# Kernel optimization log

Hardware: AMD Instinct MI355X
Metric: run time of the kernel (lower is better)

## Reference

```python
import jax, jax.numpy as jnp
import numpy as np

HEADS = 8
DIM_HEAD = 64


def setup_inputs() -> dict:
    key = jax.random.key(0)
    ks = jax.random.split(key, 6)
    dim = 512
    inner = HEADS * DIM_HEAD  # 512
    x = jax.random.normal(ks[0], (4, 4096, dim), dtype=jnp.float32)
    s = 1.0 / np.sqrt(dim)
    Wq = jax.random.normal(ks[1], (dim, inner), dtype=jnp.float32) * s
    Wk = jax.random.normal(ks[2], (dim, inner), dtype=jnp.float32) * s
    Wv = jax.random.normal(ks[3], (dim, inner), dtype=jnp.float32) * s
    Wo = jax.random.normal(ks[4], (inner, dim), dtype=jnp.float32) * (1.0 / np.sqrt(inner))
    bo = jax.random.normal(ks[5], (dim,), dtype=jnp.float32) * 0.01
    return {"x": x, "Wq": Wq, "Wk": Wk, "Wv": Wv, "Wo": Wo, "bo": bo}


def reference(x, Wq, Wk, Wv, Wo, bo):
    b, n, _ = x.shape
    h, d = HEADS, DIM_HEAD
    # project and split heads: [b, h, n, d]
    q = (x @ Wq).reshape(b, n, h, d).transpose(0, 2, 1, 3)
    k = (x @ Wk).reshape(b, n, h, d).transpose(0, 2, 1, 3)
    v = (x @ Wv).reshape(b, n, h, d).transpose(0, 2, 1, 3)
    q = jax.nn.softmax(q, axis=-1)
    k = jax.nn.softmax(k, axis=-1)
    context = jnp.einsum('bhnd,bhne->bhde', k, v)  # small d x d per head
    out = jnp.einsum('bhnd,bhde->bhne', q, context)
    out = out.transpose(0, 2, 1, 3).reshape(b, n, h * d)
    return out @ Wo + bo
```

## Files before the change

### kernel.cpp

```cpp
#include <hip/hip_runtime.h>

typedef unsigned short u16;
typedef unsigned int   u32;
typedef __bf16 bf16x8 __attribute__((ext_vector_type(8)));
typedef float  f32x4  __attribute__((ext_vector_type(4)));
typedef u16    u16x8  __attribute__((ext_vector_type(8)));
typedef u16    u16x4  __attribute__((ext_vector_type(4)));

__device__ __forceinline__ float b2f(u16 h) {
  return __builtin_bit_cast(float, ((u32)h) << 16);
}
__device__ __forceinline__ u16 f2b(float f) {
  u32 u = __builtin_bit_cast(u32, f);
  u32 r = u + 0x7FFFu + ((u >> 16) & 1u);
  return (u16)(r >> 16);
}

#define GLD_AS1(p) ((const __attribute__((address_space(1))) void*)(p))
#define LDS_AS3(p) ((__attribute__((address_space(3))) void*)(p))

__global__ void gemm_qkv_kernel(const u16* __restrict__ A, const u16* __restrict__ Bt,
                                u16* __restrict__ qb, u16* __restrict__ kT,
                                u16* __restrict__ vT) {
  const int K = 512;
  __shared__ u16 smem[2 * 64 * 72];
  u16* As = smem;
  u16* Bs = smem + 128 * 32;
  const int id = blockIdx.x;
  const int tn = id >> 7;
  const int tm = (id & 7) * 16 + ((id >> 3) & 15);
  const int tileN = tn * 128;
  const int tileM = tm * 128;
  const int t = threadIdx.x;
  const int lane = t & 63;
  const int wave = t >> 6;
  const int mbase = (wave >> 1) * 64;
  const int nbase = (wave & 1) * 64;
  const int fm = lane & 15;
  const int kg = lane >> 4;

  f32x4 acc[4][4];
#pragma unroll
  for (int i = 0; i < 4; ++i)
#pragma unroll
    for (int j = 0; j < 4; ++j) acc[i][j] = (f32x4){0.f, 0.f, 0.f, 0.f};

  for (int k0 = 0; k0 < K; k0 += 32) {
#pragma unroll
    for (int p = 0; p < 2; ++p) {
      int c = p * 256 + t;
      int r = c >> 2;
      int g = (c & 3) ^ ((r >> 1) & 3);
      const u16* ga = A + (size_t)(tileM + r) * K + (k0 + g * 8);
      __builtin_amdgcn_global_load_lds(GLD_AS1(ga), LDS_AS3(As + c * 8), 16, 0, 0);
      const u16* gb = Bt + (size_t)(tileN + r) * K + (k0 + g * 8);
      __builtin_amdgcn_global_load_lds(GLD_AS1(gb), LDS_AS3(Bs + c * 8), 16, 0, 0);
    }
    __syncthreads();

    bf16x8 af[4], bfr[4];
#pragma unroll
    for (int mi = 0; mi < 4; ++mi) {
      int m = mbase + mi * 16 + fm;
      int sg = kg ^ ((m >> 1) & 3);
      af[mi] = *(const bf16x8*)(As + m * 32 + sg * 8);
    }
#pragma unroll
    for (int ni = 0; ni < 4; ++ni) {
      int n = nbase + ni * 16 + fm;
      int sg = kg ^ ((n >> 1) & 3);
      bfr[ni] = *(const bf16x8*)(Bs + n * 32 + sg * 8);
    }
#pragma unroll
    for (int mi = 0; mi < 4; ++mi)
#pragma unroll
      for (int ni = 0; ni < 4; ++ni)
        acc[mi][ni] = __builtin_amdgcn_mfma_f32_16x16x32_bf16(af[mi], bfr[ni],
                                                              acc[mi][ni], 0, 0, 0);
    __syncthreads();
  }

  const int rq = lane >> 4;
  const int region = tn >> 2;

  float inv[4][4];
  if (region <= 1) {
#pragma unroll
    for (int mi = 0; mi < 4; ++mi)
#pragma unroll
      for (int ni = 0; ni < 4; ++ni)
#pragma unroll
        for (int reg = 0; reg < 4; ++reg)
          acc[mi][ni][reg] = __expf(acc[mi][ni][reg]);
#pragma unroll
    for (int mi = 0; mi < 4; ++mi)
#pragma unroll
      for (int reg = 0; reg < 4; ++reg) {
        float s = acc[mi][0][reg] + acc[mi][1][reg] + acc[mi][2][reg] + acc[mi][3][reg];
        s += __shfl_xor(s, 1);
        s += __shfl_xor(s, 2);
        s += __shfl_xor(s, 4);
        s += __shfl_xor(s, 8);
        inv[mi][reg] = 1.f / s;
      }
  } else {
#pragma unroll
    for (int mi = 0; mi < 4; ++mi)
#pragma unroll
      for (int reg = 0; reg < 4; ++reg) inv[mi][reg] = 1.f;
  }

  if (region == 0) {
#pragma unroll
    for (int mi = 0; mi < 4; ++mi)
#pragma unroll
      for (int ni = 0; ni < 4; ++ni)
#pragma unroll
        for (int reg = 0; reg < 4; ++reg) {
          int gr = tileM + mbase + mi * 16 + rq * 4 + reg;
          int gc = tileN + nbase + ni * 16 + fm;
          qb[(size_t)gr * 512 + gc] = f2b(acc[mi][ni][reg] * inv[mi][reg]);
        }
  }

  u16* scw = smem + (wave & 1) * (64 * 72);
  u16* base = (region == 1) ? kT : vT;
  const int hd = tileN + nbase - ((region == 1) ? 512 : 1024);
  const int gr0 = tileM + mbase;
  const int bh = (gr0 >> 12) * 8 + (hd >> 6);
  const int n0 = gr0 & 4095;

  auto transpose_store = [&]() {
#pragma unroll
    for (int mi = 0; mi < 4; ++mi)
#pragma unroll
      for (int ni = 0; ni < 4; ++ni) {
        u16x4 o;
#pragma unroll
        for (int reg = 0; reg < 4; ++reg)
          o[reg] = f2b(acc[mi][ni][reg] * inv[mi][reg]);
        *(u16x4*)(scw + (ni * 16 + fm) * 72 + mi * 16 + rq * 4) = o;
      }
#pragma unroll
    for (int i = 0; i < 8; ++i) {
      int row = i * 8 + (lane >> 3);
      int seg = lane & 7;
      u16x8 val = *(const u16x8*)(scw + row * 72 + seg * 8);
      *(u16x8*)(base + ((size_t)bh * 64 + row) * 4096 + n0 + seg * 8) = val;
    }
  };

  if (region != 0 && wave < 2) transpose_store();
  __syncthreads();
  if (region != 0 && wave >= 2) transpose_store();
}

__global__ void prep_all_kernel(const float* __restrict__ x, const float* __restrict__ Wq,
                                const float* __restrict__ Wk, const float* __restrict__ Wv,
                                const float* __restrict__ Wo, u16* __restrict__ xb,
                                u16* __restrict__ Wt, u16* __restrict__ Wot) {
  __shared__ u16 tr[64 * 72];
  const int id = blockIdx.x;
  const int t = threadIdx.x;

  if (id < 4096) {
    int i = (id * 256 + t) * 8;
    float4 a = *(const float4*)(x + i);
    float4 b = *(const float4*)(x + i + 4);
    u16x8 o;
    o[0] = f2b(a.x); o[1] = f2b(a.y); o[2] = f2b(a.z); o[3] = f2b(a.w);
    o[4] = f2b(b.x); o[5] = f2b(b.y); o[6] = f2b(b.z); o[7] = f2b(b.w);
    *(u16x8*)(xb + i) = o;
    return;
  }
  const float* W;
  u16* dst;
  int n0, k0;
  if (id < 4288) {
    int tile = id - 4096;
    n0 = (tile >> 3) * 64;
    k0 = (tile & 7) * 64;
    W = (n0 < 512) ? Wq : ((n0 < 1024) ? Wk : Wv);
    dst = Wt;
  } else {
    int tile = id - 4288;
    n0 = (tile >> 3) * 64;
    k0 = (tile & 7) * 64;
    W = Wo;
    dst = Wot;
  }
  int cin = (n0 & 511);
  int c = t & 63;
  int r0 = t >> 6;
#pragma unroll
  for (int i = 0; i < 16; ++i) {
    int r = r0 * 16 + i;
    tr[c * 72 + r] = f2b(W[(size_t)(k0 + r) * 512 + cin + c]);
  }
  __syncthreads();
#pragma unroll
  for (int j = 0; j < 2; ++j) {
    int idx = j * 256 + t;
    int row = idx >> 3;
    int seg = idx & 7;
    u16x8 val = *(const u16x8*)(tr + row * 72 + seg * 8);
    *(u16x8*)(dst + (size_t)(n0 + row) * 512 + k0 + seg * 8) = val;
  }
}

__global__ void context_kernel(const u16* __restrict__ kT, const u16* __restrict__ vT,
                               float* __restrict__ ctxp) {
  __shared__ u16 ks_lds[64 * 32];
  __shared__ u16 vs_lds[64 * 32];
  const int bh = blockIdx.x;
  const int s = blockIdx.y;
  const int t = threadIdx.x;
  const int lane = t & 63;
  const int wave = t >> 6;
  const int fm = lane & 15;
  const int kg = lane >> 4;

  const u16* kbase = kT + (size_t)bh * 64 * 4096;
  const u16* vbase = vT + (size_t)bh * 64 * 4096;
  const int r = t >> 2;
  const int slot = t & 3;
  const int g = slot ^ ((r >> 1) & 3);
  const size_t goff = (size_t)r * 4096 + s * 256 + g * 8;

  f32x4 acc[4];
#pragma unroll
  for (int i = 0; i < 4; ++i) acc[i] = (f32x4){0.f, 0.f, 0.f, 0.f};

  for (int ki = 0; ki < 8; ++ki) {
    __builtin_amdgcn_global_load_lds(GLD_AS1(vbase + goff + ki * 32),
                                     LDS_AS3(vs_lds + t * 8), 16, 0, 0);
    __builtin_amdgcn_global_load_lds(GLD_AS1(kbase + goff + ki * 32),
                                     LDS_AS3(ks_lds + t * 8), 16, 0, 0);
    __syncthreads();
    int d = wave * 16 + fm;
    bf16x8 af = *(const bf16x8*)(ks_lds + d * 32 + (kg ^ ((d >> 1) & 3)) * 8);
#pragma unroll
    for (int et = 0; et < 4; ++et) {
      int e = et * 16 + fm;
      bf16x8 bfr = *(const bf16x8*)(vs_lds + e * 32 + (kg ^ ((e >> 1) & 3)) * 8);
      acc[et] = __builtin_amdgcn_mfma_f32_16x16x32_bf16(af, bfr, acc[et], 0, 0, 0);
    }
    __syncthreads();
  }

  const int rq = lane >> 4;
  float* cp = ctxp + ((size_t)s * 32 + bh) * 4096;
#pragma unroll
  for (int et = 0; et < 4; ++et)
#pragma unroll
    for (int reg = 0; reg < 4; ++reg)
      cp[(wave * 16 + rq * 4 + reg) * 64 + et * 16 + fm] = acc[et][reg];
}

__global__ void ctxm_kernel(const float* __restrict__ ctxp, const u16* __restrict__ Wot,
                            u16* __restrict__ Mt) {
  __shared__ u16 ctxd[64 * 72];
  const int bh = blockIdx.x;
  const int b = bh >> 3, h = bh & 7;
  const int t = threadIdx.x;
  const int lane = t & 63;
  const int wave = t >> 6;
  const int fm = lane & 15;
  const int kg = lane >> 4;
  const int rq = lane >> 4;

#pragma unroll
  for (int it = 0; it < 4; ++it) {
    int idx = it * 1024 + t * 4;
    f32x4 s = (f32x4){0.f, 0.f, 0.f, 0.f};
#pragma unroll
    for (int p = 0; p < 16; ++p)
      s += *(const f32x4*)(ctxp + ((size_t)p * 32 + bh) * 4096 + idx);
    u16x4 o;
#pragma unroll
    for (int j = 0; j < 4; ++j) o[j] = f2b(s[j]);
    int d = idx >> 6, e = idx & 63;
    *(u16x4*)(ctxd + d * 72 + e) = o;
  }
  __syncthreads();

  f32x4 acc[8][4];
#pragma unroll
  for (int i = 0; i < 8; ++i)
#pragma unroll
    for (int j = 0; j < 4; ++j) acc[i][j] = (f32x4){0.f, 0.f, 0.f, 0.f};

#pragma unroll
  for (int ks = 0; ks < 2; ++ks) {
    bf16x8 bfr[4];
#pragma unroll
    for (int dt = 0; dt < 4; ++dt)
      bfr[dt] = *(const bf16x8*)(ctxd + (dt * 16 + fm) * 72 + ks * 32 + kg * 8);
#pragma unroll
    for (int mi = 0; mi < 8; ++mi) {
      int c = wave * 128 + mi * 16 + fm;
      bf16x8 af = *(const bf16x8*)(Wot + (size_t)c * 512 + h * 64 + ks * 32 + kg * 8);
#pragma unroll
      for (int dt = 0; dt < 4; ++dt)
        acc[mi][dt] = __builtin_amdgcn_mfma_f32_16x16x32_bf16(af, bfr[dt],
                                                              acc[mi][dt], 0, 0, 0);
    }
  }

  u16* mb = Mt + (size_t)b * 512 * 512;
#pragma unroll
  for (int mi = 0; mi < 8; ++mi)
#pragma unroll
    for (int dt = 0; dt < 4; ++dt)
#pragma unroll
      for (int reg = 0; reg < 4; ++reg) {
        int c = wave * 128 + mi * 16 + rq * 4 + reg;
        mb[(size_t)c * 512 + h * 64 + dt * 16 + fm] = f2b(acc[mi][dt][reg]);
      }
}

__global__ void gemm_out_kernel(const u16* __restrict__ A, const u16* __restrict__ Mt,
                                float* __restrict__ Cout, const float* __restrict__ bias) {
  const int K = 512, N = 512;
  __shared__ u16 As[128 * 32];
  __shared__ u16 Bs[128 * 32];
  const int id = blockIdx.x;
  const int tn = id >> 7;
  const int tm = (id & 7) * 16 + ((id >> 3) & 15);
  const int tileN = tn * 128;
  const int tileM = tm * 128;
  const u16* Bt = Mt + (size_t)(tm >> 5) * 512 * 512;
  const int t = threadIdx.x;
  const int lane = t & 63;
  const int wave = t >> 6;
  const int mbase = (wave >> 1) * 64;
  const int nbase = (wave & 1) * 64;
  const int fm = lane & 15;
  const int kg = lane >> 4;

  f32x4 acc[4][4];
#pragma unroll
  for (int i = 0; i < 4; ++i)
#pragma unroll
    for (int j = 0; j < 4; ++j) acc[i][j] = (f32x4){0.f, 0.f, 0.f, 0.f};

  for (int k0 = 0; k0 < K; k0 += 32) {
#pragma unroll
    for (int p = 0; p < 2; ++p) {
      int c = p * 256 + t;
      int r = c >> 2;
      int g = (c & 3) ^ ((r >> 1) & 3);
      const u16* ga = A + (size_t)(tileM + r) * K + (k0 + g * 8);
      __builtin_amdgcn_global_load_lds(GLD_AS1(ga), LDS_AS3(As + c * 8), 16, 0, 0);
      const u16* gb = Bt + (size_t)(tileN + r) * K + (k0 + g * 8);
      __builtin_amdgcn_global_load_lds(GLD_AS1(gb), LDS_AS3(Bs + c * 8), 16, 0, 0);
    }
    __syncthreads();

    bf16x8 af[4], bfr[4];
#pragma unroll
    for (int mi = 0; mi < 4; ++mi) {
      int m = mbase + mi * 16 + fm;
      int sg = kg ^ ((m >> 1) & 3);
      af[mi] = *(const bf16x8*)(As + m * 32 + sg * 8);
    }
#pragma unroll
    for (int ni = 0; ni < 4; ++ni) {
      int n = nbase + ni * 16 + fm;
      int sg = kg ^ ((n >> 1) & 3);
      bfr[ni] = *(const bf16x8*)(Bs + n * 32 + sg * 8);
    }
#pragma unroll
    for (int mi = 0; mi < 4; ++mi)
#pragma unroll
      for (int ni = 0; ni < 4; ++ni)
        acc[mi][ni] = __builtin_amdgcn_mfma_f32_16x16x32_bf16(af[mi], bfr[ni],
                                                              acc[mi][ni], 0, 0, 0);
    __syncthreads();
  }

  const int rq = lane >> 4;
#pragma unroll
  for (int mi = 0; mi < 4; ++mi)
#pragma unroll
    for (int ni = 0; ni < 4; ++ni)
#pragma unroll
      for (int reg = 0; reg < 4; ++reg) {
        int gr = tileM + mbase + mi * 16 + rq * 4 + reg;
        int gc = tileN + nbase + ni * 16 + fm;
        Cout[(size_t)gr * N + gc] = acc[mi][ni][reg] + bias[gc];
      }
}

extern "C" void kernel_launch(void* const* d_in, const int* in_sizes, int n_in,
                              void* d_out, int out_size, void* d_ws, size_t ws_size,
                              hipStream_t stream) {
  const float* x  = (const float*)d_in[0];
  const float* Wq = (const float*)d_in[1];
  const float* Wk = (const float*)d_in[2];
  const float* Wv = (const float*)d_in[3];
  const float* Wo = (const float*)d_in[4];
  const float* bo = (const float*)d_in[5];

  char* w = (char*)d_ws;
  u16* xb   = (u16*)w;    w += (size_t)16384 * 512 * 2;
  u16* Wt   = (u16*)w;    w += (size_t)1536 * 512 * 2;
  u16* Wot  = (u16*)w;    w += (size_t)512 * 512 * 2;
  u16* qbuf = (u16*)w;    w += (size_t)16384 * 512 * 2;
  u16* kT   = (u16*)w;    w += (size_t)32 * 64 * 4096 * 2;
  u16* vT   = (u16*)w;    w += (size_t)32 * 64 * 4096 * 2;
  float* ctxp = (float*)w; w += (size_t)16 * 32 * 4096 * 4;
  u16* Mt   = (u16*)w;    w += (size_t)4 * 512 * 512 * 2;

  prep_all_kernel<<<4352, 256, 0, stream>>>(x, Wq, Wk, Wv, Wo, xb, Wt, Wot);
  gemm_qkv_kernel<<<1536, 256, 0, stream>>>(xb, Wt, qbuf, kT, vT);
  context_kernel<<<dim3(32, 16), 256, 0, stream>>>(kT, vT, ctxp);
  ctxm_kernel<<<32, 256, 0, stream>>>(ctxp, Wot, Mt);
  gemm_out_kernel<<<512, 256, 0, stream>>>(qbuf, Mt, (float*)d_out, bo);
}
```

Before: 172.7 us.

## Fuse K^T V context computation into QKV GEMM epilogue

The K/V blocks of the QKV GEMM now load one head's K columns and the matching V columns into a single 128-wide tile. They apply softmax to K and compute the per-tile partial K^T V context with MFMA directly from LDS, writing fp32 partials per 128-row chunk. This removes the kT/vT transposed global writes and the separate context kernel along with its reloads. In exchange the reduction in ctxm doubles to 32 partials and the ctxp buffer grows.

```diff
diff --git a/kernel.cpp b/kernel.cpp
--- a/kernel.cpp
+++ b/kernel.cpp
@@ -20,8 +20,7 @@
 #define LDS_AS3(p) ((__attribute__((address_space(3))) void*)(p))
 
 __global__ void gemm_qkv_kernel(const u16* __restrict__ A, const u16* __restrict__ Bt,
-                                u16* __restrict__ qb, u16* __restrict__ kT,
-                                u16* __restrict__ vT) {
+                                u16* __restrict__ qb, float* __restrict__ ctxp) {
   const int K = 512;
   __shared__ u16 smem[2 * 64 * 72];
   u16* As = smem;
@@ -29,7 +28,6 @@
   const int id = blockIdx.x;
   const int tn = id >> 7;
   const int tm = (id & 7) * 16 + ((id >> 3) & 15);
-  const int tileN = tn * 128;
   const int tileM = tm * 128;
   const int t = threadIdx.x;
   const int lane = t & 63;
@@ -38,12 +36,14 @@
   const int nbase = (wave & 1) * 64;
   const int fm = lane & 15;
   const int kg = lane >> 4;
+  const bool is_q = (tn < 4);
+  const int j = tn - 4;
 
   f32x4 acc[4][4];
 #pragma unroll
   for (int i = 0; i < 4; ++i)
 #pragma unroll
-    for (int j = 0; j < 4; ++j) acc[i][j] = (f32x4){0.f, 0.f, 0.f, 0.f};
+    for (int jj = 0; jj < 4; ++jj) acc[i][jj] = (f32x4){0.f, 0.f, 0.f, 0.f};
 
   for (int k0 = 0; k0 < K; k0 += 32) {
 #pragma unroll
@@ -53,7 +53,8 @@
       int g = (c & 3) ^ ((r >> 1) & 3);
       const u16* ga = A + (size_t)(tileM + r) * K + (k0 + g * 8);
       __builtin_amdgcn_global_load_lds(GLD_AS1(ga), LDS_AS3(As + c * 8), 16, 0, 0);
-      const u16* gb = Bt + (size_t)(tileN + r) * K + (k0 + g * 8);
+      int brow = is_q ? (tn * 128 + r) : (512 + j * 64 + r + (r >> 6) * 448);
+      const u16* gb = Bt + (size_t)brow * K + (k0 + g * 8);
       __builtin_amdgcn_global_load_lds(GLD_AS1(gb), LDS_AS3(Bs + c * 8), 16, 0, 0);
     }
     __syncthreads();
@@ -81,10 +82,10 @@
   }
 
   const int rq = lane >> 4;
-  const int region = tn >> 2;
 
   float inv[4][4];
-  if (region <= 1) {
+  const bool do_sm = is_q || ((wave & 1) == 0);
+  if (do_sm) {
 #pragma unroll
     for (int mi = 0; mi < 4; ++mi)
 #pragma unroll
@@ -110,7 +111,7 @@
       for (int reg = 0; reg < 4; ++reg) inv[mi][reg] = 1.f;
   }
 
-  if (region == 0) {
+  if (is_q) {
 #pragma unroll
     for (int mi = 0; mi < 4; ++mi)
 #pragma unroll
@@ -118,41 +119,53 @@
 #pragma unroll
         for (int reg = 0; reg < 4; ++reg) {
           int gr = tileM + mbase + mi * 16 + rq * 4 + reg;
-          int gc = tileN + nbase + ni * 16 + fm;
+          int gc = tn * 128 + nbase + ni * 16 + fm;
           qb[(size_t)gr * 512 + gc] = f2b(acc[mi][ni][reg] * inv[mi][reg]);
         }
-  }
-
-  u16* scw = smem + (wave & 1) * (64 * 72);
-  u16* base = (region == 1) ? kT : vT;
-  const int hd = tileN + nbase - ((region == 1) ? 512 : 1024);
-  const int gr0 = tileM + mbase;
-  const int bh = (gr0 >> 12) * 8 + (hd >> 6);
-  const int n0 = gr0 & 4095;
-
-  auto transpose_store = [&]() {
-#pragma unroll
-    for (int mi = 0; mi < 4; ++mi)
-#pragma unroll
-      for (int ni = 0; ni < 4; ++ni) {
-        u16x4 o;
-#pragma unroll
-        for (int reg = 0; reg < 4; ++reg)
-          o[reg] = f2b(acc[mi][ni][reg] * inv[mi][reg]);
-        *(u16x4*)(scw + (ni * 16 + fm) * 72 + mi * 16 + rq * 4) = o;
+    return;
+  }
+
+  u16* T = smem;
+  f32x4 cacc[4];
+#pragma unroll
+  for (int i = 0; i < 4; ++i) cacc[i] = (f32x4){0.f, 0.f, 0.f, 0.f};
+
+#pragma unroll
+  for (int ph = 0; ph < 2; ++ph) {
+    if ((wave >> 1) == ph) {
+#pragma unroll
+      for (int mi = 0; mi < 4; ++mi)
+#pragma unroll
+        for (int ni = 0; ni < 4; ++ni) {
+          u16x4 o;
+#pragma unroll
+          for (int reg = 0; reg < 4; ++reg)
+            o[reg] = f2b(acc[mi][ni][reg] * inv[mi][reg]);
+          int c = nbase + ni * 16 + fm;
+          *(u16x4*)(T + c * 72 + mi * 16 + rq * 4) = o;
+        }
+    }
+    __syncthreads();
+#pragma unroll
+    for (int kk = 0; kk < 2; ++kk) {
+      bf16x8 afc = *(const bf16x8*)(T + (wave * 16 + fm) * 72 + kk * 32 + kg * 8);
+#pragma unroll
+      for (int et = 0; et < 4; ++et) {
+        bf16x8 bfc = *(const bf16x8*)(T + (64 + et * 16 + fm) * 72 + kk * 32 + kg * 8);
+        cacc[et] = __builtin_amdgcn_mfma_f32_16x16x32_bf16(afc, bfc, cacc[et], 0, 0, 0);
       }
-#pragma unroll
-    for (int i = 0; i < 8; ++i) {
-      int row = i * 8 + (lane >> 3);
-      int seg = lane & 7;
-      u16x8 val = *(const u16x8*)(scw + row * 72 + seg * 8);
-      *(u16x8*)(base + ((size_t)bh * 64 + row) * 4096 + n0 + seg * 8) = val;
-    }
-  };
-
-  if (region != 0 && wave < 2) transpose_store();
-  __syncthreads();
-  if (region != 0 && wave >= 2) transpose_store();
+    }
+    __syncthreads();
+  }
+
+  const int b = tm >> 5;
+  const int s = tm & 31;
+  float* cp = ctxp + ((size_t)s * 32 + b * 8 + j) * 4096;
+#pragma unroll
+  for (int et = 0; et < 4; ++et)
+#pragma unroll
+    for (int reg = 0; reg < 4; ++reg)
+      cp[(wave * 16 + rq * 4 + reg) * 64 + et * 16 + fm] = cacc[et][reg];
 }
 
 __global__ void prep_all_kernel(const float* __restrict__ x, const float* __restrict__ Wq,
@@ -199,62 +212,13 @@
   }
   __syncthreads();
 #pragma unroll
-  for (int j = 0; j < 2; ++j) {
-    int idx = j * 256 + t;
+  for (int jj = 0; jj < 2; ++jj) {
+    int idx = jj * 256 + t;
     int row = idx >> 3;
     int seg = idx & 7;
     u16x8 val = *(const u16x8*)(tr + row * 72 + seg * 8);
     *(u16x8*)(dst + (size_t)(n0 + row) * 512 + k0 + seg * 8) = val;
   }
-}
-
-__global__ void context_kernel(const u16* __restrict__ kT, const u16* __restrict__ vT,
-                               float* __restrict__ ctxp) {
-  __shared__ u16 ks_lds[64 * 32];
-  __shared__ u16 vs_lds[64 * 32];
-  const int bh = blockIdx.x;
-  const int s = blockIdx.y;
-  const int t = threadIdx.x;
-  const int lane = t & 63;
-  const int wave = t >> 6;
-  const int fm = lane & 15;
-  const int kg = lane >> 4;
-
-  const u16* kbase = kT + (size_t)bh * 64 * 4096;
-  const u16* vbase = vT + (size_t)bh * 64 * 4096;
-  const int r = t >> 2;
-  const int slot = t & 3;
-  const int g = slot ^ ((r >> 1) & 3);
-  const size_t goff = (size_t)r * 4096 + s * 256 + g * 8;
-
-  f32x4 acc[4];
-#pragma unroll
-  for (int i = 0; i < 4; ++i) acc[i] = (f32x4){0.f, 0.f, 0.f, 0.f};
-
-  for (int ki = 0; ki < 8; ++ki) {
-    __builtin_amdgcn_global_load_lds(GLD_AS1(vbase + goff + ki * 32),
-                                     LDS_AS3(vs_lds + t * 8), 16, 0, 0);
-    __builtin_amdgcn_global_load_lds(GLD_AS1(kbase + goff + ki * 32),
-                                     LDS_AS3(ks_lds + t * 8), 16, 0, 0);
-    __syncthreads();
-    int d = wave * 16 + fm;
-    bf16x8 af = *(const bf16x8*)(ks_lds + d * 32 + (kg ^ ((d >> 1) & 3)) * 8);
-#pragma unroll
-    for (int et = 0; et < 4; ++et) {
-      int e = et * 16 + fm;
-      bf16x8 bfr = *(const bf16x8*)(vs_lds + e * 32 + (kg ^ ((e >> 1) & 3)) * 8);
-      acc[et] = __builtin_amdgcn_mfma_f32_16x16x32_bf16(af, bfr, acc[et], 0, 0, 0);
-    }
-    __syncthreads();
-  }
-
-  const int rq = lane >> 4;
-  float* cp = ctxp + ((size_t)s * 32 + bh) * 4096;
-#pragma unroll
-  for (int et = 0; et < 4; ++et)
-#pragma unroll
-    for (int reg = 0; reg < 4; ++reg)
-      cp[(wave * 16 + rq * 4 + reg) * 64 + et * 16 + fm] = acc[et][reg];
 }
 
 __global__ void ctxm_kernel(const float* __restrict__ ctxp, const u16* __restrict__ Wot,
@@ -274,11 +238,11 @@
     int idx = it * 1024 + t * 4;
     f32x4 s = (f32x4){0.f, 0.f, 0.f, 0.f};
 #pragma unroll
-    for (int p = 0; p < 16; ++p)
+    for (int p = 0; p < 32; ++p)
       s += *(const f32x4*)(ctxp + ((size_t)p * 32 + bh) * 4096 + idx);
     u16x4 o;
 #pragma unroll
-    for (int j = 0; j < 4; ++j) o[j] = f2b(s[j]);
+    for (int jj = 0; jj < 4; ++jj) o[jj] = f2b(s[jj]);
     int d = idx >> 6, e = idx & 63;
     *(u16x4*)(ctxd + d * 72 + e) = o;
   }
@@ -288,7 +252,7 @@
 #pragma unroll
   for (int i = 0; i < 8; ++i)
 #pragma unroll
-    for (int j = 0; j < 4; ++j) acc[i][j] = (f32x4){0.f, 0.f, 0.f, 0.f};
+    for (int jj = 0; jj < 4; ++jj) acc[i][jj] = (f32x4){0.f, 0.f, 0.f, 0.f};
 
 #pragma unroll
   for (int ks = 0; ks < 2; ++ks) {
@@ -342,7 +306,7 @@
 #pragma unroll
   for (int i = 0; i < 4; ++i)
 #pragma unroll
-    for (int j = 0; j < 4; ++j) acc[i][j] = (f32x4){0.f, 0.f, 0.f, 0.f};
+    for (int jj = 0; jj < 4; ++jj) acc[i][jj] = (f32x4){0.f, 0.f, 0.f, 0.f};
 
   for (int k0 = 0; k0 < K; k0 += 32) {
 #pragma unroll
@@ -407,14 +371,11 @@
   u16* Wt   = (u16*)w;    w += (size_t)1536 * 512 * 2;
   u16* Wot  = (u16*)w;    w += (size_t)512 * 512 * 2;
   u16* qbuf = (u16*)w;    w += (size_t)16384 * 512 * 2;
-  u16* kT   = (u16*)w;    w += (size_t)32 * 64 * 4096 * 2;
-  u16* vT   = (u16*)w;    w += (size_t)32 * 64 * 4096 * 2;
-  float* ctxp = (float*)w; w += (size_t)16 * 32 * 4096 * 4;
+  float* ctxp = (float*)w; w += (size_t)32 * 32 * 4096 * 4;
   u16* Mt   = (u16*)w;    w += (size_t)4 * 512 * 512 * 2;
 
   prep_all_kernel<<<4352, 256, 0, stream>>>(x, Wq, Wk, Wv, Wo, xb, Wt, Wot);
-  gemm_qkv_kernel<<<1536, 256, 0, stream>>>(xb, Wt, qbuf, kT, vT);
-  context_kernel<<<dim3(32, 16), 256, 0, stream>>>(kT, vT, ctxp);
+  gemm_qkv_kernel<<<1536, 256, 0, stream>>>(xb, Wt, qbuf, ctxp);
   ctxm_kernel<<<32, 256, 0, stream>>>(ctxp, Wot, Mt);
   gemm_out_kernel<<<512, 256, 0, stream>>>(qbuf, Mt, (float*)d_out, bo);
 }
```

Result: slower. 192.2 us (+11.3%).
